# Performance work log

Hardware: AMD Instinct MI355X
Metric: run time of the kernel (lower is better)

## Reference

```python
import jax, jax.numpy as jnp
import numpy as np

N_LAYERS = 2
D_CONV = 4
D_MODEL = 768
D_INNER = 1536
D_STATE = 16
D_DELTA = 48
B = 2
L = 1024
EPS = 1e-5


def setup_inputs() -> dict:
    key = jax.random.key(0)
    ks = jax.random.split(key, 8)
    s = 0.02
    x = jax.random.normal(ks[0], (B, L, D_MODEL), jnp.float32)
    in_proj_w = jax.random.normal(ks[1], (N_LAYERS, 2 * D_INNER, D_MODEL), jnp.float32) * s
    conv_w = jax.random.normal(ks[2], (N_LAYERS, D_INNER, 1, D_CONV), jnp.float32) * s
    conv_b = jnp.zeros((N_LAYERS, D_INNER), jnp.float32)
    xproj_w = jax.random.normal(ks[3], (N_LAYERS, D_DELTA + 2 * D_STATE, D_INNER), jnp.float32) * s
    dt_w = jax.random.normal(ks[4], (N_LAYERS, D_INNER, D_DELTA), jnp.float32) * s
    dt_b = jax.random.normal(ks[5], (N_LAYERS, D_INNER), jnp.float32) * s
    A_log = jnp.tile(jnp.log(jnp.arange(1, D_STATE + 1, dtype=jnp.float32)), (N_LAYERS, D_INNER, 1))
    D = jnp.ones((N_LAYERS, D_INNER), jnp.float32)
    out_proj_w = jax.random.normal(ks[6], (N_LAYERS, D_MODEL, D_INNER), jnp.float32) * s
    norm_w = jnp.ones((N_LAYERS, D_MODEL), jnp.float32)
    return dict(x=x, in_proj_w=in_proj_w, conv_w=conv_w, conv_b=conv_b,
                xproj_w=xproj_w, dt_w=dt_w, dt_b=dt_b, A_log=A_log, D=D,
                out_proj_w=out_proj_w, norm_w=norm_w)


def rms_norm(x, w):
    return w * x * jax.lax.rsqrt(jnp.mean(x * x, axis=-1, keepdims=True) + EPS)


def causal_depthwise_conv(x, w, b):
    # x: [B, L, D_INNER], w: [D_INNER, 1, K], b: [D_INNER]
    xc = x.transpose(0, 2, 1)  # [B, D, L]
    y = jax.lax.conv_general_dilated(
        xc, w, window_strides=(1,), padding=[(D_CONV - 1, 0)],
        dimension_numbers=("NCH", "OIH", "NCH"), feature_group_count=D_INNER)
    y = y + b[None, :, None]
    return y.transpose(0, 2, 1)  # [B, L, D]


def ssm(x, A_log, D, xproj_w, dt_w, dt_b):
    # x: [B, L, D_INNER]
    A = -jnp.exp(A_log)  # [D, N]
    dbc = jnp.einsum('bld,ed->ble', x, xproj_w)
    delta, Bc, C = jnp.split(dbc, [D_DELTA, D_DELTA + D_STATE], axis=-1)
    delta = jax.nn.softplus(jnp.einsum('blr,dr->bld', delta, dt_w) + dt_b)  # [B, L, D]
    dA = jnp.exp(delta[..., None] * A)                          # [B, L, D, N]
    dBx = delta[..., None] * Bc[:, :, None, :] * x[..., None]   # [B, L, D, N]

    def step(h, inp):
        dA_t, dBx_t, C_t = inp
        h = dA_t * h + dBx_t                      # [B, D, N]
        y = jnp.einsum('bdn,bn->bd', h, C_t)      # [B, D]
        return h, y

    h0 = jnp.zeros((x.shape[0], D_INNER, D_STATE), x.dtype)
    _, ys = jax.lax.scan(step, h0, (dA.transpose(1, 0, 2, 3),
                                    dBx.transpose(1, 0, 2, 3),
                                    C.transpose(1, 0, 2)))
    y = ys.transpose(1, 0, 2)  # [B, L, D]
    return y + D * x


def mamba_block(x, in_w, cw, cb, xp_w, dtw, dtb, Alog, Dp, out_w):
    xz = jnp.einsum('blm,em->ble', x, in_w)           # [B, L, 2*D_INNER]
    xi, z = jnp.split(xz, 2, axis=-1)
    xi = jax.nn.silu(causal_depthwise_conv(xi, cw, cb))
    y = ssm(xi, Alog, Dp, xp_w, dtw, dtb)
    out = y * jax.nn.silu(z)
    return jnp.einsum('bld,md->blm', out, out_w)


def reference(x, in_proj_w, conv_w, conv_b, xproj_w, dt_w, dt_b, A_log, D, out_proj_w, norm_w):
    for i in range(N_LAYERS):
        x = x + mamba_block(rms_norm(x, norm_w[i]), in_proj_w[i], conv_w[i], conv_b[i],
                            xproj_w[i], dt_w[i], dt_b[i], A_log[i], D[i], out_proj_w[i])
    return x
```

## Files before the change

### kernel.cpp

```cpp
#include <hip/hip_runtime.h>
#include <hip/hip_bf16.h>
#include <cstdint>

#define NL 2
#define DM 768
#define DI 1536
#define DS 16
#define DD 48
#define DCONV 4
#define BB 2
#define LL 1024
#define MROWS (BB*LL)
#define DBCW (DD + 2*DS)
#define TC 32
#define NCH (LL/TC)
#define KSPL 4
#define XPN 128

typedef __bf16 bf16x8 __attribute__((ext_vector_type(8)));
typedef float f32x4 __attribute__((ext_vector_type(4)));
typedef ushort ushort8 __attribute__((ext_vector_type(8)));
using bf16 = __hip_bfloat16;

__device__ __forceinline__ float softplusf(float x) {
  return (x > 20.f) ? x : log1pf(__expf(x));
}

__device__ __forceinline__ float bfu2f(ushort u) {
  return __uint_as_float((uint32_t)u << 16);
}

__device__ __forceinline__ ushort f2bfu(float f) {
  const bf16 h = __float2bfloat16(f);
  return *reinterpret_cast<const ushort*>(&h);
}

__device__ __forceinline__ void load_lds16(const void* g, void* l) {
  __builtin_amdgcn_global_load_lds(
      (const __attribute__((address_space(1))) void*)g,
      (__attribute__((address_space(3))) void*)l, 16, 0, 0);
}

#define WI_N (NL*2*DI*DM)
#define WX_N (NL*XPN*DI)
#define WD_N (NL*DI*DD)
#define WO_N (NL*DM*DI)
__global__ __launch_bounds__(256)
void prep_weights(const float* __restrict__ wi, const float* __restrict__ wx,
                  const float* __restrict__ wd, const float* __restrict__ wo,
                  bf16* __restrict__ bi, bf16* __restrict__ bx,
                  bf16* __restrict__ bd, bf16* __restrict__ bo)
{
  int i = blockIdx.x * 256 + threadIdx.x;
  if (i < WI_N) { bi[i] = __float2bfloat16(wi[i]); return; }
  i -= WI_N;
  if (i < WX_N) {
    const int l = i / (XPN*DI), r = (i / DI) % XPN, k = i % DI;
    const float v = (r < DBCW) ? wx[((size_t)l*DBCW + r)*DI + k] : 0.f;
    bx[i] = __float2bfloat16(v); return;
  }
  i -= WX_N;
  if (i < WD_N) { bd[i] = __float2bfloat16(wd[i]); return; }
  i -= WD_N;
  if (i < WO_N) { bo[i] = __float2bfloat16(wo[i]); }
}

__global__ __launch_bounds__(256)
void rmsnorm_kernel(const float* __restrict__ x, const float* __restrict__ w,
                    bf16* __restrict__ out)
{
  const int row = blockIdx.x;
  const float* xr = x + (size_t)row * DM;
  const int t = threadIdx.x;
  float v0 = xr[t], v1 = xr[t + 256], v2 = xr[t + 512];
  float ss = v0*v0 + v1*v1 + v2*v2;
  #pragma unroll
  for (int off = 32; off > 0; off >>= 1) ss += __shfl_down(ss, off);
  __shared__ float sred[4];
  if ((t & 63) == 0) sred[t >> 6] = ss;
  __syncthreads();
  const float scale = rsqrtf((sred[0]+sred[1]+sred[2]+sred[3]) * (1.f/DM) + 1e-5f);
  out[(size_t)row*DM + t      ] = __float2bfloat16(v0 * scale * w[t]);
  out[(size_t)row*DM + t + 256] = __float2bfloat16(v1 * scale * w[t + 256]);
  out[(size_t)row*DM + t + 512] = __float2bfloat16(v2 * scale * w[t + 512]);
}

__global__ __launch_bounds__(256)
void gemm_in128(const bf16* __restrict__ A, const bf16* __restrict__ W,
                bf16* __restrict__ xb, bf16* __restrict__ zb)
{
  __shared__ __align__(16) bf16 As[2][128][32];
  __shared__ __align__(16) bf16 Ws[2][128][32];
  const int tid = threadIdx.x;
  const int wave = tid >> 6, lane = tid & 63;
  const int m0 = blockIdx.x * 128, n0 = blockIdx.y * 128;
  const int wr = (wave >> 1) * 64, wc = (wave & 1) * 64;
  const int l16 = lane & 15, quad = lane >> 4;
  const int srow = wave * 16 + (lane >> 2);
  const int scol = (lane & 3) * 8;

  f32x4 acc[4][4] = {};

  for (int k0 = 0; k0 < DM; k0 += 64) {
    #pragma unroll
    for (int kk = 0; kk < 2; ++kk) {
      load_lds16(A + (size_t)(m0 + srow) * DM + k0 + kk*32 + scol,      &As[kk][wave*16][0]);
      load_lds16(A + (size_t)(m0 + 64 + srow) * DM + k0 + kk*32 + scol, &As[kk][64 + wave*16][0]);
      load_lds16(W + (size_t)(n0 + srow) * DM + k0 + kk*32 + scol,      &Ws[kk][wave*16][0]);
      load_lds16(W + (size_t)(n0 + 64 + srow) * DM + k0 + kk*32 + scol, &Ws[kk][64 + wave*16][0]);
    }
    __syncthreads();

    #pragma unroll
    for (int kk = 0; kk < 2; ++kk) {
      bf16x8 af[4], wf[4];
      #pragma unroll
      for (int i = 0; i < 4; ++i)
        af[i] = *reinterpret_cast<const bf16x8*>(&As[kk][wr + i*16 + l16][quad*8]);
      #pragma unroll
      for (int j = 0; j < 4; ++j)
        wf[j] = *reinterpret_cast<const bf16x8*>(&Ws[kk][wc + j*16 + l16][quad*8]);
      #pragma unroll
      for (int i = 0; i < 4; ++i)
        #pragma unroll
        for (int j = 0; j < 4; ++j)
          acc[i][j] = __builtin_amdgcn_mfma_f32_16x16x32_bf16(af[i], wf[j], acc[i][j], 0, 0, 0);
    }
    __syncthreads();
  }

  const bool isz = (n0 >= DI);
  #pragma unroll
  for (int i = 0; i < 4; ++i) {
    #pragma unroll
    for (int j = 0; j < 4; ++j) {
      const int col = n0 + wc + j*16 + l16;
      #pragma unroll
      for (int r = 0; r < 4; ++r) {
        const int row = m0 + wr + i*16 + quad*4 + r;
        const float v = acc[i][j][r];
        if (!isz) xb[(size_t)row*DI + col]      = __float2bfloat16(v);
        else      zb[(size_t)row*DI + col - DI] = __float2bfloat16(v);
      }
    }
  }
}

template<int MODE>
__global__ __launch_bounds__(256)
void gemm64l(const bf16* __restrict__ A, int lda,
             const bf16* __restrict__ W, int ldw,
             float* __restrict__ C, int ldc, int N, int K,
             const float* __restrict__ res)
{
  __shared__ __align__(16) bf16 As[2][64][32];
  __shared__ __align__(16) bf16 Ws[2][64][32];
  const int tid = threadIdx.x;
  const int wave = tid >> 6, lane = tid & 63;
  const int m0 = blockIdx.x * 64, n0 = blockIdx.y * 64;
  const int wr = (wave >> 1) * 32, wc = (wave & 1) * 32;
  const int l16 = lane & 15, quad = lane >> 4;
  const int srow = wave * 16 + (lane >> 2);
  const int scol = (lane & 3) * 8;

  A += (size_t)blockIdx.z * K;
  W += (size_t)blockIdx.z * K;
  C += (size_t)blockIdx.z * MROWS * ldc;

  f32x4 acc[2][2] = {};

  for (int k0 = 0; k0 < K; k0 += 64) {
    #pragma unroll
    for (int kk = 0; kk < 2; ++kk) {
      load_lds16(A + (size_t)(m0 + srow) * lda + k0 + kk*32 + scol, &As[kk][wave*16][0]);
      load_lds16(W + (size_t)(n0 + srow) * ldw + k0 + kk*32 + scol, &Ws[kk][wave*16][0]);
    }
    __syncthreads();
    #pragma unroll
    for (int kk = 0; kk < 2; ++kk) {
      bf16x8 af[2], wf[2];
      #pragma unroll
      for (int i = 0; i < 2; ++i)
        af[i] = *reinterpret_cast<const bf16x8*>(&As[kk][wr + i*16 + l16][quad*8]);
      #pragma unroll
      for (int j = 0; j < 2; ++j)
        wf[j] = *reinterpret_cast<const bf16x8*>(&Ws[kk][wc + j*16 + l16][quad*8]);
      #pragma unroll
      for (int i = 0; i < 2; ++i)
        #pragma unroll
        for (int j = 0; j < 2; ++j)
          acc[i][j] = __builtin_amdgcn_mfma_f32_16x16x32_bf16(af[i], wf[j], acc[i][j], 0, 0, 0);
    }
    __syncthreads();
  }

  #pragma unroll
  for (int i = 0; i < 2; ++i) {
    #pragma unroll
    for (int j = 0; j < 2; ++j) {
      const int col = n0 + wc + j*16 + l16;
      if (col >= N) continue;
      #pragma unroll
      for (int r = 0; r < 4; ++r) {
        const int row = m0 + wr + i*16 + quad*4 + r;
        float v = acc[i][j][r];
        const size_t idx = (size_t)row * ldc + col;
        if (MODE == 3) v += res[idx];
        C[idx] = v;
      }
    }
  }
}

__global__ __launch_bounds__(256)
void conv_silu_kernel(const bf16* __restrict__ xb, const float* __restrict__ cw,
                      const float* __restrict__ cb, bf16* __restrict__ xob)
{
  const int idx = blockIdx.x * 256 + threadIdx.x;
  const int d8 = idx % (DI/8);
  const int row = idx / (DI/8);
  const int l = row % LL;
  const int d0 = d8 * 8;

  float4 cwv[8];
  #pragma unroll
  for (int j = 0; j < 8; ++j)
    cwv[j] = reinterpret_cast<const float4*>(cw)[d0 + j];

  float acc[8];
  {
    const float4* cbp = reinterpret_cast<const float4*>(cb + d0);
    float4 c0 = cbp[0], c1 = cbp[1];
    acc[0]=c0.x; acc[1]=c0.y; acc[2]=c0.z; acc[3]=c0.w;
    acc[4]=c1.x; acc[5]=c1.y; acc[6]=c1.z; acc[7]=c1.w;
  }
  #pragma unroll
  for (int k = 0; k < DCONV; ++k) {
    const int ll = l - (DCONV-1) + k;
    if (ll >= 0) {
      const ushort8 v = *reinterpret_cast<const ushort8*>(
          xb + (size_t)(row - (DCONV-1) + k) * DI + d0);
      #pragma unroll
      for (int j = 0; j < 8; ++j) {
        const float w = (k==0) ? cwv[j].x : (k==1) ? cwv[j].y : (k==2) ? cwv[j].z : cwv[j].w;
        acc[j] += w * bfu2f(v[j]);
      }
    }
  }
  ushort8 o;
  #pragma unroll
  for (int j = 0; j < 8; ++j) {
    const float s = acc[j] / (1.f + __expf(-acc[j]));
    o[j] = f2bfu(s);
  }
  *reinterpret_cast<ushort8*>(xob + (size_t)row*DI + d0) = o;
}

__global__ __launch_bounds__(256)
void gemm_dt(const float* __restrict__ xpart, const bf16* __restrict__ W,
             bf16* __restrict__ Cb, const float* __restrict__ bias)
{
  __shared__ __align__(16) bf16 As[64][40];
  __shared__ __align__(16) bf16 Ws[64][40];
  const int tid = threadIdx.x;
  const int m0 = blockIdx.x * 64, n0 = blockIdx.y * 64;
  const int wave = tid >> 6, lane = tid & 63;
  const int wr = (wave >> 1) * 32, wc = (wave & 1) * 32;
  const int l16 = lane & 15, quad = lane >> 4;
  const int srow = tid >> 2;
  const int scol = (tid & 3) * 8;

  f32x4 acc[2][2] = {};

  #pragma unroll
  for (int k0 = 0; k0 < DD; k0 += 32) {
    {
      const int cbase = k0 + scol;
      bf16* dst = &As[srow][scol];
      if (cbase < DD) {
        float a[8] = {0,0,0,0,0,0,0,0};
        #pragma unroll
        for (int z = 0; z < KSPL; ++z) {
          const float4* p = reinterpret_cast<const float4*>(
              xpart + (size_t)z*MROWS*DBCW + (size_t)(m0 + srow)*DBCW + cbase);
          const float4 u = p[0], v = p[1];
          a[0]+=u.x; a[1]+=u.y; a[2]+=u.z; a[3]+=u.w;
          a[4]+=v.x; a[5]+=v.y; a[6]+=v.z; a[7]+=v.w;
        }
        #pragma unroll
        for (int j = 0; j < 8; ++j) dst[j] = __float2bfloat16(a[j]);
      } else {
        *reinterpret_cast<uint4*>(dst) = make_uint4(0,0,0,0);
      }
    }
    {
      const bf16* src = W + (size_t)(n0 + srow) * DD + (k0 + scol);
      bf16* dst = &Ws[srow][scol];
      if (k0 + scol + 8 <= DD) {
        *reinterpret_cast<uint4*>(dst) = *reinterpret_cast<const uint4*>(src);
      } else {
        #pragma unroll
        for (int j = 0; j < 8; ++j)
          dst[j] = (k0 + scol + j < DD) ? src[j] : __float2bfloat16(0.f);
      }
    }
    __syncthreads();
    bf16x8 af[2], wf[2];
    #pragma unroll
    for (int i = 0; i < 2; ++i)
      af[i] = *reinterpret_cast<const bf16x8*>(&As[wr + i*16 + l16][quad*8]);
    #pragma unroll
    for (int j = 0; j < 2; ++j)
      wf[j] = *reinterpret_cast<const bf16x8*>(&Ws[wc + j*16 + l16][quad*8]);
    #pragma unroll
    for (int i = 0; i < 2; ++i)
      #pragma unroll
      for (int j = 0; j < 2; ++j)
        acc[i][j] = __builtin_amdgcn_mfma_f32_16x16x32_bf16(af[i], wf[j], acc[i][j], 0, 0, 0);
    __syncthreads();
  }

  #pragma unroll
  for (int i = 0; i < 2; ++i) {
    #pragma unroll
    for (int j = 0; j < 2; ++j) {
      const int col = n0 + wc + j*16 + l16;
      #pragma unroll
      for (int r = 0; r < 4; ++r) {
        const int row = m0 + wr + i*16 + quad*4 + r;
        Cb[(size_t)row*DI + col] = __float2bfloat16(softplusf(acc[i][j][r] + bias[col]));
      }
    }
  }
}

__global__ __launch_bounds__(256)
void scan_pass1(const bf16* __restrict__ delta, const bf16* __restrict__ xi,
                const float* __restrict__ xpart, const float* __restrict__ A_log,
                float* __restrict__ sdl_out, float* __restrict__ H)
{
  __shared__ float Bs[TC][DS];
  __shared__ __align__(16) ushort Dl[TC][128];
  __shared__ __align__(16) ushort Xl[TC][128];
  const int tid = threadIdx.x;
  const int wave = tid >> 6, lane = tid & 63;
  const int s = lane >> 5;
  const int dloc = wave*32 + (lane & 31);
  const int dt = blockIdx.x % (DI/128);
  const int c  = (blockIdx.x / (DI/128)) % NCH;
  const int b  =  blockIdx.x / ((DI/128)*NCH);
  const int d  = dt*128 + dloc;
  const int t0 = c*TC;

  {
    const int rsub = lane >> 4;
    const int csub = (lane & 15) * 8;
    const size_t g0 = ((size_t)b*LL + t0 + wave*8 + rsub)*DI + dt*128 + csub;
    load_lds16(delta + g0,                 &Dl[wave*8][0]);
    load_lds16(delta + g0 + (size_t)4*DI,  &Dl[wave*8+4][0]);
    load_lds16(xi + g0,                    &Xl[wave*8][0]);
    load_lds16(xi + g0 + (size_t)4*DI,     &Xl[wave*8+4][0]);
  }

  for (int i = tid; i < TC*DS; i += 256) {
    const int t = i >> 4, n = i & 15;
    const size_t rb = ((size_t)b*LL + t0 + t)*DBCW + DD + n;
    float v = xpart[rb];
    #pragma unroll
    for (int z = 1; z < KSPL; ++z) v += xpart[rb + (size_t)z*(MROWS*DBCW)];
    Bs[t][n] = v;
  }

  float An[8];
  {
    const float4* ap = (const float4*)(A_log + (size_t)d*DS + s*8);
    float4 v0 = ap[0], v1 = ap[1];
    An[0] = -__expf(v0.x)*1.44269504f; An[1] = -__expf(v0.y)*1.44269504f;
    An[2] = -__expf(v0.z)*1.44269504f; An[3] = -__expf(v0.w)*1.44269504f;
    An[4] = -__expf(v1.x)*1.44269504f; An[5] = -__expf(v1.y)*1.44269504f;
    An[6] = -__expf(v1.z)*1.44269504f; An[7] = -__expf(v1.w)*1.44269504f;
  }
  __syncthreads();

  float h[8] = {0.f,0.f,0.f,0.f,0.f,0.f,0.f,0.f};
  float sacc = 0.f;
  #pragma unroll
  for (int t = 0; t < TC; ++t) {
    const float dl = bfu2f(Dl[t][dloc]);
    const float xv = bfu2f(Xl[t][dloc]);
    const float dlxv = dl * xv;
    sacc += dl;
    const float4* brow = (const float4*)&Bs[t][s*8];
    const float4 b0 = brow[0], b1 = brow[1];
    const float bb[8] = {b0.x,b0.y,b0.z,b0.w,b1.x,b1.y,b1.z,b1.w};
    #pragma unroll
    for (int n = 0; n < 8; ++n) {
      const float dA = exp2f(dl * An[n]);
      h[n] = dA*h[n] + dlxv*bb[n];
    }
  }
  const size_t base = (((size_t)b*NCH + c)*DI + d)*DS + s*8;
  float4* Hp = (float4*)(H + base);
  Hp[0] = make_float4(h[0],h[1],h[2],h[3]);
  Hp[1] = make_float4(h[4],h[5],h[6],h[7]);
  if (s == 0) sdl_out[((size_t)b*NCH + c)*DI + d] = sacc;
}

__global__ __launch_bounds__(256)
void scan_fix(const float* __restrict__ sdl, const float* __restrict__ A_log,
              float* __restrict__ H)
{
  const int idx = blockIdx.x * 256 + threadIdx.x;
  const int n = idx & 15;
  const int d = (idx >> 4) % DI;
  const int b = idx / (DS * DI);
  const float An = -__expf(A_log[(size_t)d*DS + n]) * 1.44269504f;
  float hin = 0.f;
  #pragma unroll 8
  for (int c = 0; c < NCH; ++c) {
    const float Pv = exp2f(An * sdl[((size_t)b*NCH + c)*DI + d]);
    const size_t ic = (((size_t)b*NCH + c)*DI + d)*DS + n;
    const float Hv = H[ic];
    H[ic] = hin;
    hin = fmaf(Pv, hin, Hv);
  }
}

__global__ __launch_bounds__(256)
void scan_pass2(const bf16* __restrict__ delta, const bf16* __restrict__ xi,
                const float* __restrict__ xpart, const float* __restrict__ A_log,
                const float* __restrict__ H, const float* __restrict__ Dp,
                const bf16* __restrict__ zb, bf16* __restrict__ outb)
{
  __shared__ float Bs[TC][DS];
  __shared__ float Cs[TC][DS];
  __shared__ __align__(16) ushort Dl[TC][128];
  __shared__ __align__(16) ushort Xl[TC][128];
  __shared__ __align__(16) ushort Zl[TC][128];
  const int tid = threadIdx.x;
  const int wave = tid >> 6, lane = tid & 63;
  const int s = lane >> 5;
  const int dloc = wave*32 + (lane & 31);
  const int dt = blockIdx.x % (DI/128);
  const int c  = (blockIdx.x / (DI/128)) % NCH;
  const int b  =  blockIdx.x / ((DI/128)*NCH);
  const int d  = dt*128 + dloc;
  const int t0 = c*TC;

  {
    const int rsub = lane >> 4;
    const int csub = (lane & 15) * 8;
    const size_t g0 = ((size_t)b*LL + t0 + wave*8 + rsub)*DI + dt*128 + csub;
    load_lds16(delta + g0,                 &Dl[wave*8][0]);
    load_lds16(delta + g0 + (size_t)4*DI,  &Dl[wave*8+4][0]);
    load_lds16(xi + g0,                    &Xl[wave*8][0]);
    load_lds16(xi + g0 + (size_t)4*DI,     &Xl[wave*8+4][0]);
    load_lds16(zb + g0,                    &Zl[wave*8][0]);
    load_lds16(zb + g0 + (size_t)4*DI,     &Zl[wave*8+4][0]);
  }

  for (int i = tid; i < TC*2*DS; i += 256) {
    const int t = i >> 5, n32 = i & 31;
    const size_t rb = ((size_t)b*LL + t0 + t)*DBCW + DD + n32;
    float v = xpart[rb];
    #pragma unroll
    for (int z = 1; z < KSPL; ++z) v += xpart[rb + (size_t)z*(MROWS*DBCW)];
    if (n32 < DS) Bs[t][n32] = v;
    else          Cs[t][n32 - DS] = v;
  }

  float An[8];
  {
    const float4* ap = (const float4*)(A_log + (size_t)d*DS + s*8);
    float4 v0 = ap[0], v1 = ap[1];
    An[0] = -__expf(v0.x)*1.44269504f; An[1] = -__expf(v0.y)*1.44269504f;
    An[2] = -__expf(v0.z)*1.44269504f; An[3] = -__expf(v0.w)*1.44269504f;
    An[4] = -__expf(v1.x)*1.44269504f; An[5] = -__expf(v1.y)*1.44269504f;
    An[6] = -__expf(v1.z)*1.44269504f; An[7] = -__expf(v1.w)*1.44269504f;
  }
  const float Dd = Dp[d];
  float h[8];
  {
    const float4* hp = (const float4*)(H + (((size_t)b*NCH + c)*DI + d)*DS + s*8);
    float4 h0 = hp[0], h1 = hp[1];
    h[0]=h0.x; h[1]=h0.y; h[2]=h0.z; h[3]=h0.w;
    h[4]=h1.x; h[5]=h1.y; h[6]=h1.z; h[7]=h1.w;
  }
  __syncthreads();

  bf16* optr = outb + ((size_t)b*LL + t0)*DI + d;

  #pragma unroll
  for (int t = 0; t < TC; ++t) {
    const float dl = bfu2f(Dl[t][dloc]);
    const float xv = bfu2f(Xl[t][dloc]);
    const float zv = bfu2f(Zl[t][dloc]);
    const float dlxv = dl * xv;
    const float4* brow = (const float4*)&Bs[t][s*8];
    const float4* crow = (const float4*)&Cs[t][s*8];
    const float4 b0 = brow[0], b1 = brow[1];
    const float4 c0 = crow[0], c1 = crow[1];
    const float bb[8] = {b0.x,b0.y,b0.z,b0.w,b1.x,b1.y,b1.z,b1.w};
    const float cc[8] = {c0.x,c0.y,c0.z,c0.w,c1.x,c1.y,c1.z,c1.w};
    float y = 0.f;
    #pragma unroll
    for (int n = 0; n < 8; ++n) {
      const float dA = exp2f(dl * An[n]);
      h[n] = dA*h[n] + dlxv*bb[n];
      y = fmaf(h[n], cc[n], y);
    }
    y += __shfl_xor(y, 32);
    if (s == 0) {
      const float o = (y + Dd * xv) * (zv / (1.f + __expf(-zv)));
      optr[(size_t)t*DI] = __float2bfloat16(o);
    }
  }
}

extern "C" void kernel_launch(void* const* d_in, const int* in_sizes, int n_in,
                              void* d_out, int out_size, void* d_ws, size_t ws_size,
                              hipStream_t stream)
{
  const float* x_in   = (const float*)d_in[0];
  const float* w_inp  = (const float*)d_in[1];
  const float* w_conv = (const float*)d_in[2];
  const float* b_conv = (const float*)d_in[3];
  const float* w_xprj = (const float*)d_in[4];
  const float* w_dtp  = (const float*)d_in[5];
  const float* b_dt   = (const float*)d_in[6];
  const float* a_log  = (const float*)d_in[7];
  const float* d_par  = (const float*)d_in[8];
  const float* w_outp = (const float*)d_in[9];
  const float* w_norm = (const float*)d_in[10];
  float* xfinal = (float*)d_out;

  char* ws = (char*)d_ws;
  size_t off = 0;
  auto alloc = [&](size_t bytes) -> void* {
    void* p = ws + off;
    off += (bytes + 255) & ~(size_t)255;
    return p;
  };
  bf16*  wb_in  = (bf16*) alloc((size_t)WI_N*2);
  bf16*  wb_xp  = (bf16*) alloc((size_t)WX_N*2);
  bf16*  wb_dt  = (bf16*) alloc((size_t)WD_N*2);
  bf16*  wb_out = (bf16*) alloc((size_t)WO_N*2);
  bf16*  xn     = (bf16*) alloc((size_t)MROWS*DM*2);
  bf16*  xb     = (bf16*) alloc((size_t)MROWS*DI*2);
  bf16*  zb     = (bf16*) alloc((size_t)MROWS*DI*2);
  bf16*  xcb    = (bf16*) alloc((size_t)MROWS*DI*2);
  float* xpart  = (float*)alloc((size_t)KSPL*MROWS*DBCW*4);
  bf16*  dltb   = (bf16*) alloc((size_t)MROWS*DI*2);
  bf16*  scb    = (bf16*) alloc((size_t)MROWS*DI*2);
  float* x1     = (float*)alloc((size_t)MROWS*DM*4);
  float* sdlw   = (float*)alloc((size_t)BB*NCH*DI*4);
  float* Hws    = (float*)alloc((size_t)BB*NCH*DI*DS*4);

  prep_weights<<<(WI_N+WX_N+WD_N+WO_N + 255)/256, 256, 0, stream>>>(
      w_inp, w_xprj, w_dtp, w_outp, wb_in, wb_xp, wb_dt, wb_out);

  const float* xprev = x_in;
  for (int l = 0; l < NL; ++l) {
    rmsnorm_kernel<<<MROWS, 256, 0, stream>>>(xprev, w_norm + l*DM, xn);

    gemm_in128<<<dim3(MROWS/128, (2*DI)/128), 256, 0, stream>>>(
        xn, wb_in + (size_t)l*2*DI*DM, xb, zb);

    conv_silu_kernel<<<(MROWS*DI/8)/256, 256, 0, stream>>>(
        xb, w_conv + l*DI*DCONV, b_conv + l*DI, xcb);

    gemm64l<0><<<dim3(MROWS/64, XPN/64, KSPL), 256, 0, stream>>>(
        xcb, DI, wb_xp + (size_t)l*XPN*DI, DI, xpart, DBCW, DBCW, DI/KSPL, nullptr);

    gemm_dt<<<dim3(MROWS/64, DI/64), 256, 0, stream>>>(
        xpart, wb_dt + (size_t)l*DI*DD, dltb, b_dt + l*DI);

    scan_pass1<<<BB*NCH*(DI/128), 256, 0, stream>>>(
        dltb, xcb, xpart, a_log + (size_t)l*DI*DS, sdlw, Hws);
    scan_fix<<<(BB*DI*DS)/256, 256, 0, stream>>>(
        sdlw, a_log + (size_t)l*DI*DS, Hws);
    scan_pass2<<<BB*NCH*(DI/128), 256, 0, stream>>>(
        dltb, xcb, xpart, a_log + (size_t)l*DI*DS, Hws, d_par + l*DI, zb, scb);

    float* xout = (l == NL-1) ? xfinal : x1;
    gemm64l<3><<<dim3(MROWS/64, DM/64, 1), 256, 0, stream>>>(
        scb, DI, wb_out + (size_t)l*DM*DI, DI, xout, DM, DM, DI, xprev);

    xprev = x1;
  }
}
```

Baseline: 355.3 us.

## Fold chunk-carry fixup into scan_pass2 by recomputing prefix state per chunk

Removes the separate scan_fix kernel that sequentially propagated inter-chunk states. Each scan_pass2 block now rebuilds its incoming hidden state by looping over all preceding chunk summaries (H and summed delta) and applying the decay recurrence itself. This saves one kernel launch and the serial fix pass per layer. In exchange it adds redundant work that grows with chunk index (up to 31 iterations of 8 exp2 and loads per thread), which loads later chunks more than earlier ones.

```diff
diff --git a/kernel.cpp b/kernel.cpp
--- a/kernel.cpp
+++ b/kernel.cpp
@@ -407,29 +407,10 @@
 }
 
 __global__ __launch_bounds__(256)
-void scan_fix(const float* __restrict__ sdl, const float* __restrict__ A_log,
-              float* __restrict__ H)
-{
-  const int idx = blockIdx.x * 256 + threadIdx.x;
-  const int n = idx & 15;
-  const int d = (idx >> 4) % DI;
-  const int b = idx / (DS * DI);
-  const float An = -__expf(A_log[(size_t)d*DS + n]) * 1.44269504f;
-  float hin = 0.f;
-  #pragma unroll 8
-  for (int c = 0; c < NCH; ++c) {
-    const float Pv = exp2f(An * sdl[((size_t)b*NCH + c)*DI + d]);
-    const size_t ic = (((size_t)b*NCH + c)*DI + d)*DS + n;
-    const float Hv = H[ic];
-    H[ic] = hin;
-    hin = fmaf(Pv, hin, Hv);
-  }
-}
-
-__global__ __launch_bounds__(256)
 void scan_pass2(const bf16* __restrict__ delta, const bf16* __restrict__ xi,
                 const float* __restrict__ xpart, const float* __restrict__ A_log,
-                const float* __restrict__ H, const float* __restrict__ Dp,
+                const float* __restrict__ H, const float* __restrict__ sdl,
+                const float* __restrict__ Dp,
                 const bf16* __restrict__ zb, bf16* __restrict__ outb)
 {
   __shared__ float Bs[TC][DS];
@@ -479,12 +460,20 @@
     An[6] = -__expf(v1.z)*1.44269504f; An[7] = -__expf(v1.w)*1.44269504f;
   }
   const float Dd = Dp[d];
-  float h[8];
+
+  float h[8] = {0.f,0.f,0.f,0.f,0.f,0.f,0.f,0.f};
   {
-    const float4* hp = (const float4*)(H + (((size_t)b*NCH + c)*DI + d)*DS + s*8);
-    float4 h0 = hp[0], h1 = hp[1];
-    h[0]=h0.x; h[1]=h0.y; h[2]=h0.z; h[3]=h0.w;
-    h[4]=h1.x; h[5]=h1.y; h[6]=h1.z; h[7]=h1.w;
+    const size_t hb = ((size_t)b*NCH*DI + d)*DS + s*8;
+    const size_t sb = (size_t)b*NCH*DI + d;
+    for (int j = 0; j < c; ++j) {
+      const float sd = sdl[sb + (size_t)j*DI];
+      const float4* hp = (const float4*)(H + hb + (size_t)j*(DI*DS));
+      const float4 h0 = hp[0], h1 = hp[1];
+      const float Hj[8] = {h0.x,h0.y,h0.z,h0.w,h1.x,h1.y,h1.z,h1.w};
+      #pragma unroll
+      for (int n = 0; n < 8; ++n)
+        h[n] = fmaf(exp2f(An[n]*sd), h[n], Hj[n]);
+    }
   }
   __syncthreads();
 
@@ -577,10 +566,9 @@
 
     scan_pass1<<<BB*NCH*(DI/128), 256, 0, stream>>>(
         dltb, xcb, xpart, a_log + (size_t)l*DI*DS, sdlw, Hws);
-    scan_fix<<<(BB*DI*DS)/256, 256, 0, stream>>>(
-        sdlw, a_log + (size_t)l*DI*DS, Hws);
     scan_pass2<<<BB*NCH*(DI/128), 256, 0, stream>>>(
-        dltb, xcb, xpart, a_log + (size_t)l*DI*DS, Hws, d_par + l*DI, zb, scb);
+        dltb, xcb, xpart, a_log + (size_t)l*DI*DS, Hws, sdlw,
+        d_par + l*DI, zb, scb);
 
     float* xout = (l == NL-1) ? xfinal : x1;
     gemm64l<3><<<dim3(MROWS/64, DM/64, 1), 256, 0, stream>>>(
```

Result: slower. 367.9 us (+3.5%).
